# Kernel optimization log

Hardware: AMD Instinct MI355X
Metric: run time of the kernel (lower is better)

## Reference

```python
import jax, jax.numpy as jnp
import numpy as np

B, S, D_IN, D_OUT = 4, 2048, 1024, 1024


def setup_inputs() -> dict:
    key = jax.random.key(0)
    k1, k2, k3, k4 = jax.random.split(key, 4)
    scale = 1.0 / np.sqrt(D_IN)
    return {
        "x": jax.random.normal(k1, (B, S, D_IN), dtype=jnp.float32),
        # torch nn.Linear weights have shape [d_out, d_in]
        "Wq": jax.random.normal(k2, (D_OUT, D_IN), dtype=jnp.float32) * scale,
        "Wk": jax.random.normal(k3, (D_OUT, D_IN), dtype=jnp.float32) * scale,
        "Wv": jax.random.normal(k4, (D_OUT, D_IN), dtype=jnp.float32) * scale,
    }


def reference(x, Wq, Wk, Wv):
    # Linear projections (torch Linear: y = x @ W.T), no bias
    q = jnp.einsum('bsd,od->bso', x, Wq)
    k = jnp.einsum('bsd,od->bso', x, Wk)
    v = jnp.einsum('bsd,od->bso', x, Wv)
    s = q.shape[1]
    scores = jnp.einsum('bqd,bkd->bqk', q, k)  # [B, S, S]
    causal = jnp.tril(jnp.ones((s, s), dtype=bool))  # True = keep
    scores = jnp.where(causal[None], scores, -jnp.inf)
    scale = jnp.asarray(k.shape[-1], scores.dtype) ** 0.5
    weights = jax.nn.softmax(scores / scale, axis=-1)
    return jnp.einsum('bqk,bkd->bqd', weights, v)
```

## Files before the change

### kernel.cpp

```cpp
#include <hip/hip_runtime.h>

#define BATCH 4
#define SEQ   2048
#define DIM   1024
#define MTOT  (BATCH * SEQ)
#define BK    32

typedef __bf16 bf16x8 __attribute__((ext_vector_type(8)));
typedef float  f32x4  __attribute__((ext_vector_type(4)));

__device__ __forceinline__ void gl_lds16(const __bf16* g, __bf16* l) {
    __builtin_amdgcn_global_load_lds(
        (const __attribute__((address_space(1))) void*)g,
        (__attribute__((address_space(3))) void*)l,
        16, 0, 0);
}

__global__ __launch_bounds__(256) void cvt_all_kernel(
    const float* __restrict__ x,  const float* __restrict__ w0,
    const float* __restrict__ w1, const float* __restrict__ w2,
    __bf16* __restrict__ xd, __bf16* __restrict__ d0,
    __bf16* __restrict__ d1, __bf16* __restrict__ d2)
{
    const int bid = blockIdx.x;
    const float* s;
    __bf16* d;
    int base;
    if (bid < 4096)      { s = x;  d = xd; base = bid; }
    else if (bid < 4608) { s = w0; d = d0; base = bid - 4096; }
    else if (bid < 5120) { s = w1; d = d1; base = bid - 4608; }
    else                 { s = w2; d = d2; base = bid - 5120; }
    const int i = (base * 256 + threadIdx.x) * 8;
    const float4 a = *(const float4*)(s + i);
    const float4 b = *(const float4*)(s + i + 4);
    bf16x8 o;
    o[0] = (__bf16)a.x; o[1] = (__bf16)a.y; o[2] = (__bf16)a.z; o[3] = (__bf16)a.w;
    o[4] = (__bf16)b.x; o[5] = (__bf16)b.y; o[6] = (__bf16)b.z; o[7] = (__bf16)b.w;
    *(bf16x8*)(d + i) = o;
}

__device__ __forceinline__ void gemm_core(
    const __bf16* __restrict__ A, size_t lda,
    const __bf16* __restrict__ Bm, size_t ldb,
    int m0, int n0, int kTiles,
    __bf16* lA, __bf16* lB,
    f32x4 (&acc)[4][4])
{
    const int tid  = threadIdx.x;
    const int lane = tid & 63;
    const int wave = tid >> 6;
    const int wm = (wave >> 1) << 6;
    const int wn = (wave & 1) << 6;

#pragma unroll
    for (int i = 0; i < 4; ++i)
#pragma unroll
        for (int j = 0; j < 4; ++j)
            acc[i][j] = (f32x4){0.f, 0.f, 0.f, 0.f};

    for (int kt = 0; kt < kTiles; ++kt) {
        const int k0 = kt << 5;
        __syncthreads();
#pragma unroll
        for (int it = 0; it < 2; ++it) {
            const int f   = tid + (it << 8);
            const int row = f >> 2;
            const int col = (f & 3) << 3;
            gl_lds16(A  + (size_t)(m0 + row) * lda + (size_t)(k0 + col), lA + f * 8);
            gl_lds16(Bm + (size_t)(n0 + row) * ldb + (size_t)(k0 + col), lB + f * 8);
        }
        __syncthreads();

        bf16x8 af[4], bfr[4];
#pragma unroll
        for (int i = 0; i < 4; ++i) {
            af[i]  = *(const bf16x8*)(lA + (size_t)(wm + i * 16 + (lane & 15)) * BK + ((lane >> 4) << 3));
            bfr[i] = *(const bf16x8*)(lB + (size_t)(wn + i * 16 + (lane & 15)) * BK + ((lane >> 4) << 3));
        }
#pragma unroll
        for (int i = 0; i < 4; ++i)
#pragma unroll
            for (int j = 0; j < 4; ++j)
                acc[i][j] = __builtin_amdgcn_mfma_f32_16x16x32_bf16(af[i], bfr[j], acc[i][j], 0, 0, 0);
    }
}

__device__ __forceinline__ void store_tile_bf16(
    f32x4 (&acc)[4][4], __bf16* scratch, bool transpose, float scale,
    __bf16* dst, size_t ldo, size_t r0, size_t c0,
    bool expMask = false, bool diag = false)
{
    const int tid  = threadIdx.x;
    const int lane = tid & 63;
    const int wave = tid >> 6;
    const int wm = (wave >> 1) << 6, wn = (wave & 1) << 6;
    const int quad = lane >> 4;
    const int ln15 = lane & 15;

#pragma unroll
    for (int p = 0; p < 4; ++p) {
        __syncthreads();
        if (!transpose) {
            if (wm == ((p >> 1) << 6)) {
#pragma unroll
                for (int ih = 0; ih < 2; ++ih) {
                    const int i = ((p & 1) << 1) + ih;
                    const int lr = ih * 16 + quad * 4;
#pragma unroll
                    for (int j = 0; j < 4; ++j)
#pragma unroll
                        for (int r = 0; r < 4; ++r) {
                            const int lm = wm + ((p & 1) << 5) + lr + r;
                            const int ln = wn + j * 16 + ln15;
                            float v = acc[i][j][r] * scale;
                            if (expMask) {
                                v = (!diag || ln <= lm) ? __expf(v) : 0.f;
                            }
                            scratch[(lr + r) * 136 + wn + j * 16 + ln15] = (__bf16)v;
                        }
                }
            }
        } else {
            if (wn == ((p >> 1) << 6)) {
#pragma unroll
                for (int jh = 0; jh < 2; ++jh) {
                    const int j = ((p & 1) << 1) + jh;
                    const int lr = jh * 16 + ln15;
#pragma unroll
                    for (int i = 0; i < 4; ++i)
#pragma unroll
                        for (int r = 0; r < 4; ++r)
                            scratch[lr * 136 + wm + i * 16 + quad * 4 + r] =
                                (__bf16)(acc[i][j][r] * scale);
                }
            }
        }
        __syncthreads();
#pragma unroll
        for (int it = 0; it < 2; ++it) {
            const int g   = tid + (it << 8);
            const int row = g >> 4;
            const int col = (g & 15) << 3;
            *(bf16x8*)(dst + (r0 + p * 32 + row) * ldo + c0 + col) =
                *(const bf16x8*)(scratch + row * 136 + col);
        }
    }
}

__global__ __launch_bounds__(256) void qkv_kernel(
    const __bf16* __restrict__ x,
    const __bf16* __restrict__ Wq,
    const __bf16* __restrict__ Wk,
    const __bf16* __restrict__ Wv,
    __bf16* __restrict__ Q, __bf16* __restrict__ Kb, __bf16* __restrict__ Vt)
{
    __shared__ __bf16 smem[8192];
    __bf16* lA = smem;
    __bf16* lB = smem + 128 * BK;
    const int L = blockIdx.x;
    const int c = L & 7;
    const int k = L >> 3;
    const int m0 = ((c << 3) + (k / 24)) << 7;
    const int rr = k % 24;
    const int z  = rr >> 3;
    const int n0 = (rr & 7) << 7;
    const __bf16* W = (z == 0) ? Wq : (z == 1) ? Wk : Wv;

    f32x4 acc[4][4];
    gemm_core(x, DIM, W, DIM, m0, n0, DIM / BK, lA, lB, acc);

    if (z == 0) {
        store_tile_bf16(acc, smem, false, 1.f, Q,  DIM, m0, n0);
    } else if (z == 1) {
        store_tile_bf16(acc, smem, false, 1.f, Kb, DIM, m0, n0);
    } else {
        const size_t b = (size_t)(m0 >> 11), ms0 = (size_t)(m0 & (SEQ - 1));
        store_tile_bf16(acc, smem, true, 1.f, Vt + b * DIM * SEQ, SEQ, n0, ms0);
    }
}

__global__ __launch_bounds__(256) void scores_kernel(
    const __bf16* __restrict__ Q, const __bf16* __restrict__ Kb,
    __bf16* __restrict__ Sc)
{
    const int L = blockIdx.x;
    const int g = (L & 7) * 68 + (L >> 3);
    const int b = g / 136;
    const int t = g - b * 136;
    int i = (int)((sqrtf(8.f * t + 1.f) - 1.f) * 0.5f);
    while ((i + 1) * (i + 2) / 2 <= t) ++i;
    while (i * (i + 1) / 2 > t) --i;
    const int j = t - i * (i + 1) / 2;

    __shared__ __bf16 smem[8192];
    __bf16* lA = smem;
    __bf16* lB = smem + 128 * BK;
    const __bf16* A  = Q  + (size_t)b * SEQ * DIM;
    const __bf16* Bm = Kb + (size_t)b * SEQ * DIM;

    f32x4 acc[4][4];
    gemm_core(A, DIM, Bm, DIM, i << 7, j << 7, DIM / BK, lA, lB, acc);

    store_tile_bf16(acc, smem, false, 0.03125f,
                    Sc + (size_t)b * SEQ * SEQ, SEQ,
                    (size_t)(i << 7), (size_t)(j << 7),
                    true, (i == j));
}

__global__ __launch_bounds__(256) void rowsum_kernel(
    const __bf16* __restrict__ Sc, float* __restrict__ invl)
{
    const int rg = blockIdx.x;
    const int b  = rg >> 11;
    const int r  = rg & (SEQ - 1);
    const __bf16* row = Sc + ((size_t)b * SEQ + r) * SEQ;

    const int tid  = threadIdx.x;
    const int lane = tid & 63;
    const int wv   = tid >> 6;
    const int width = ((r >> 7) + 1) << 7;
    const int c0 = tid << 3;

    float s = 0.f;
    if (c0 < width) {
        const bf16x8 in = *(const bf16x8*)(row + c0);
#pragma unroll
        for (int k = 0; k < 8; ++k) s += (float)in[k];
    }
#pragma unroll
    for (int off = 32; off > 0; off >>= 1)
        s += __shfl_xor(s, off);

    __shared__ float red[4];
    if (lane == 0) red[wv] = s;
    __syncthreads();
    if (tid == 0)
        invl[rg] = 1.f / (red[0] + red[1] + red[2] + red[3]);
}

__global__ __launch_bounds__(256) void pv_kernel(
    const __bf16* __restrict__ P, const __bf16* __restrict__ Vt,
    const float* __restrict__ invl, float* __restrict__ out)
{
    const int L = blockIdx.x;
    const int c = L & 7;
    const int k = L >> 3;
    const int b = c >> 1;
    const int i = 15 - (c & 1) - ((k >> 3) << 1);
    const int x = k & 7;

    __shared__ __bf16 smem[8192];
    __bf16* lA = smem;
    __bf16* lB = smem + 128 * BK;
    const __bf16* A  = P  + (size_t)b * SEQ * SEQ;
    const __bf16* Bm = Vt + (size_t)b * DIM * SEQ;

    f32x4 acc[4][4];
    gemm_core(A, SEQ, Bm, SEQ, i << 7, x << 7, (i + 1) * (128 / BK), lA, lB, acc);

    const int lane = threadIdx.x & 63;
    const int wave = threadIdx.x >> 6;
    const int wm = (wave >> 1) << 6, wn = (wave & 1) << 6;
#pragma unroll
    for (int ii = 0; ii < 4; ++ii)
#pragma unroll
        for (int jj = 0; jj < 4; ++jj)
#pragma unroll
            for (int r = 0; r < 4; ++r) {
                const int m = (i << 7) + wm + ii * 16 + ((lane >> 4) << 2) + r;
                const int n = (x << 7) + wn + jj * 16 + (lane & 15);
                out[((size_t)b * SEQ + m) * DIM + n] =
                    acc[ii][jj][r] * invl[(b << 11) + m];
            }
}

extern "C" void kernel_launch(void* const* d_in, const int* in_sizes, int n_in,
                              void* d_out, int out_size, void* d_ws, size_t ws_size,
                              hipStream_t stream) {
    const float* x  = (const float*)d_in[0];
    const float* Wq = (const float*)d_in[1];
    const float* Wk = (const float*)d_in[2];
    const float* Wv = (const float*)d_in[3];
    float* out = (float*)d_out;

    char* ws = (char*)d_ws;
    __bf16* Q  = (__bf16*)(ws);
    __bf16* Kb = (__bf16*)(ws + (16ull << 20));
    __bf16* Vt = (__bf16*)(ws + (32ull << 20));
    __bf16* Sc = (__bf16*)(ws + (48ull << 20));
    __bf16* Wqb = (__bf16*)(ws + (80ull << 20));
    __bf16* Wkb = (__bf16*)(ws + (82ull << 20));
    __bf16* Wvb = (__bf16*)(ws + (84ull << 20));
    float*  invl = (float*)(ws + (86ull << 20));
    __bf16* xb  = (__bf16*)d_out;

    cvt_all_kernel<<<dim3(5632), 256, 0, stream>>>(x, Wq, Wk, Wv, xb, Wqb, Wkb, Wvb);

    qkv_kernel    <<<dim3(1536), 256, 0, stream>>>(xb, Wqb, Wkb, Wvb, Q, Kb, Vt);
    scores_kernel <<<dim3(544),  256, 0, stream>>>(Q, Kb, Sc);
    rowsum_kernel <<<dim3(MTOT), 256, 0, stream>>>(Sc, invl);
    pv_kernel     <<<dim3(512),  256, 0, stream>>>(Sc, Vt, invl, out);
}
```

Before: 244.5 us.

## Fuse softmax row-sum into scores epilogue via atomics, drop rowsum kernel

Removes the separate rowsum kernel, which re-read the whole lower-triangular score matrix. The row sums are now accumulated in the scores kernel's store epilogue: a shared-memory atomic reduction per 32-row slab, then global float atomics into a buffer that a new tiny kernel zeroes first. The PV kernel takes the reciprocal per row once, hoisted out of the column loop. The QKV tile order is also remapped so Q, K and V tiles are grouped by z, and the epilogue gains extra syncthreads and atomic traffic.

```diff
diff --git a/kernel.cpp b/kernel.cpp
--- a/kernel.cpp
+++ b/kernel.cpp
@@ -14,6 +14,11 @@
         (const __attribute__((address_space(1))) void*)g,
         (__attribute__((address_space(3))) void*)l,
         16, 0, 0);
+}
+
+__global__ __launch_bounds__(256) void zerol_kernel(float* __restrict__ l)
+{
+    l[blockIdx.x * 256 + threadIdx.x] = 0.f;
 }
 
 __global__ __launch_bounds__(256) void cvt_all_kernel(
@@ -85,10 +90,12 @@
     }
 }
 
+template <bool ROWSUM>
 __device__ __forceinline__ void store_tile_bf16(
     f32x4 (&acc)[4][4], __bf16* scratch, bool transpose, float scale,
     __bf16* dst, size_t ldo, size_t r0, size_t c0,
-    bool expMask = false, bool diag = false)
+    bool expMask = false, bool diag = false,
+    float* lsum = nullptr, float* gRow = nullptr)
 {
     const int tid  = threadIdx.x;
     const int lane = tid & 63;
@@ -96,6 +103,8 @@
     const int wm = (wave >> 1) << 6, wn = (wave & 1) << 6;
     const int quad = lane >> 4;
     const int ln15 = lane & 15;
+
+    if (ROWSUM && tid < 32) lsum[tid] = 0.f;
 
 #pragma unroll
     for (int p = 0; p < 4; ++p) {
@@ -141,8 +150,21 @@
             const int g   = tid + (it << 8);
             const int row = g >> 4;
             const int col = (g & 15) << 3;
-            *(bf16x8*)(dst + (r0 + p * 32 + row) * ldo + c0 + col) =
-                *(const bf16x8*)(scratch + row * 136 + col);
+            const bf16x8 vv = *(const bf16x8*)(scratch + row * 136 + col);
+            *(bf16x8*)(dst + (r0 + p * 32 + row) * ldo + c0 + col) = vv;
+            if (ROWSUM) {
+                float part = 0.f;
+#pragma unroll
+                for (int k = 0; k < 8; ++k) part += (float)vv[k];
+                atomicAdd(&lsum[row], part);
+            }
+        }
+        if (ROWSUM) {
+            __syncthreads();
+            if (tid < 32) {
+                atomicAdd(&gRow[r0 + p * 32 + tid], lsum[tid]);
+                lsum[tid] = 0.f;
+            }
         }
     }
 }
@@ -160,28 +182,28 @@
     const int L = blockIdx.x;
     const int c = L & 7;
     const int k = L >> 3;
-    const int m0 = ((c << 3) + (k / 24)) << 7;
-    const int rr = k % 24;
-    const int z  = rr >> 3;
-    const int n0 = (rr & 7) << 7;
+    const int z  = k >> 6;
+    const int p  = (k >> 3) & 7;
+    const int n0 = (k & 7) << 7;
+    const int m0 = ((c << 3) + p) << 7;
     const __bf16* W = (z == 0) ? Wq : (z == 1) ? Wk : Wv;
 
     f32x4 acc[4][4];
     gemm_core(x, DIM, W, DIM, m0, n0, DIM / BK, lA, lB, acc);
 
     if (z == 0) {
-        store_tile_bf16(acc, smem, false, 1.f, Q,  DIM, m0, n0);
+        store_tile_bf16<false>(acc, smem, false, 1.f, Q,  DIM, m0, n0);
     } else if (z == 1) {
-        store_tile_bf16(acc, smem, false, 1.f, Kb, DIM, m0, n0);
+        store_tile_bf16<false>(acc, smem, false, 1.f, Kb, DIM, m0, n0);
     } else {
         const size_t b = (size_t)(m0 >> 11), ms0 = (size_t)(m0 & (SEQ - 1));
-        store_tile_bf16(acc, smem, true, 1.f, Vt + b * DIM * SEQ, SEQ, n0, ms0);
+        store_tile_bf16<false>(acc, smem, true, 1.f, Vt + b * DIM * SEQ, SEQ, n0, ms0);
     }
 }
 
 __global__ __launch_bounds__(256) void scores_kernel(
     const __bf16* __restrict__ Q, const __bf16* __restrict__ Kb,
-    __bf16* __restrict__ Sc)
+    __bf16* __restrict__ Sc, float* __restrict__ l)
 {
     const int L = blockIdx.x;
     const int g = (L & 7) * 68 + (L >> 3);
@@ -193,6 +215,7 @@
     const int j = t - i * (i + 1) / 2;
 
     __shared__ __bf16 smem[8192];
+    __shared__ float lsum[32];
     __bf16* lA = smem;
     __bf16* lB = smem + 128 * BK;
     const __bf16* A  = Q  + (size_t)b * SEQ * DIM;
@@ -201,46 +224,16 @@
     f32x4 acc[4][4];
     gemm_core(A, DIM, Bm, DIM, i << 7, j << 7, DIM / BK, lA, lB, acc);
 
-    store_tile_bf16(acc, smem, false, 0.03125f,
-                    Sc + (size_t)b * SEQ * SEQ, SEQ,
-                    (size_t)(i << 7), (size_t)(j << 7),
-                    true, (i == j));
-}
-
-__global__ __launch_bounds__(256) void rowsum_kernel(
-    const __bf16* __restrict__ Sc, float* __restrict__ invl)
-{
-    const int rg = blockIdx.x;
-    const int b  = rg >> 11;
-    const int r  = rg & (SEQ - 1);
-    const __bf16* row = Sc + ((size_t)b * SEQ + r) * SEQ;
-
-    const int tid  = threadIdx.x;
-    const int lane = tid & 63;
-    const int wv   = tid >> 6;
-    const int width = ((r >> 7) + 1) << 7;
-    const int c0 = tid << 3;
-
-    float s = 0.f;
-    if (c0 < width) {
-        const bf16x8 in = *(const bf16x8*)(row + c0);
-#pragma unroll
-        for (int k = 0; k < 8; ++k) s += (float)in[k];
-    }
-#pragma unroll
-    for (int off = 32; off > 0; off >>= 1)
-        s += __shfl_xor(s, off);
-
-    __shared__ float red[4];
-    if (lane == 0) red[wv] = s;
-    __syncthreads();
-    if (tid == 0)
-        invl[rg] = 1.f / (red[0] + red[1] + red[2] + red[3]);
+    store_tile_bf16<true>(acc, smem, false, 0.03125f,
+                          Sc + (size_t)b * SEQ * SEQ, SEQ,
+                          (size_t)(i << 7), (size_t)(j << 7),
+                          true, (i == j),
+                          lsum, l + (b << 11));
 }
 
 __global__ __launch_bounds__(256) void pv_kernel(
     const __bf16* __restrict__ P, const __bf16* __restrict__ Vt,
-    const float* __restrict__ invl, float* __restrict__ out)
+    const float* __restrict__ l, float* __restrict__ out)
 {
     const int L = blockIdx.x;
     const int c = L & 7;
@@ -262,16 +255,18 @@
     const int wave = threadIdx.x >> 6;
     const int wm = (wave >> 1) << 6, wn = (wave & 1) << 6;
 #pragma unroll
-    for (int ii = 0; ii < 4; ++ii)
-#pragma unroll
-        for (int jj = 0; jj < 4; ++jj)
-#pragma unroll
-            for (int r = 0; r < 4; ++r) {
-                const int m = (i << 7) + wm + ii * 16 + ((lane >> 4) << 2) + r;
+    for (int ii = 0; ii < 4; ++ii) {
+#pragma unroll
+        for (int r = 0; r < 4; ++r) {
+            const int m = (i << 7) + wm + ii * 16 + ((lane >> 4) << 2) + r;
+            const float inv = 1.f / l[(b << 11) + m];
+#pragma unroll
+            for (int jj = 0; jj < 4; ++jj) {
                 const int n = (x << 7) + wn + jj * 16 + (lane & 15);
-                out[((size_t)b * SEQ + m) * DIM + n] =
-                    acc[ii][jj][r] * invl[(b << 11) + m];
-            }
+                out[((size_t)b * SEQ + m) * DIM + n] = acc[ii][jj][r] * inv;
+            }
+        }
+    }
 }
 
 extern "C" void kernel_launch(void* const* d_in, const int* in_sizes, int n_in,
@@ -291,13 +286,13 @@
     __bf16* Wqb = (__bf16*)(ws + (80ull << 20));
     __bf16* Wkb = (__bf16*)(ws + (82ull << 20));
     __bf16* Wvb = (__bf16*)(ws + (84ull << 20));
-    float*  invl = (float*)(ws + (86ull << 20));
+    float*  l   = (float*)(ws + (86ull << 20));
     __bf16* xb  = (__bf16*)d_out;
 
+    zerol_kernel  <<<dim3(32),   256, 0, stream>>>(l);
     cvt_all_kernel<<<dim3(5632), 256, 0, stream>>>(x, Wq, Wk, Wv, xb, Wqb, Wkb, Wvb);
 
     qkv_kernel    <<<dim3(1536), 256, 0, stream>>>(xb, Wqb, Wkb, Wvb, Q, Kb, Vt);
-    scores_kernel <<<dim3(544),  256, 0, stream>>>(Q, Kb, Sc);
-    rowsum_kernel <<<dim3(MTOT), 256, 0, stream>>>(Sc, invl);
-    pv_kernel     <<<dim3(512),  256, 0, stream>>>(Sc, Vt, invl, out);
-}
+    scores_kernel <<<dim3(544),  256, 0, stream>>>(Q, Kb, Sc, l);
+    pv_kernel     <<<dim3(512),  256, 0, stream>>>(Sc, Vt, l, out);
+}
```

Result: no change. 247.4 us (+1.2%).
